# Kernel optimization log

Hardware: AMD Instinct MI355X
Metric: run time of the kernel (lower is better)

The kernel has to match this reference:

```python
import jax, jax.numpy as jnp
import numpy as np

B, R, T, F_IN, L, D, H, OUT, ES = 8, 128, 64, 32, 64, 64, 128, 32, 2048
DT = 0.1  # dt_step from init


def _glorot(key, shape):
    scale = 1.0 / np.sqrt(shape[0])
    return (jax.random.normal(key, shape, jnp.float32) * scale).astype(jnp.float32)


def setup_inputs() -> dict:
    key = jax.random.key(0)
    ks = jax.random.split(key, 20)
    return {
        "node_feats": jax.random.normal(ks[0], (B, R, T, F_IN), jnp.float32),
        "eps": jax.random.normal(ks[1], (B, R, L + D), jnp.float32),
        "space_w": jax.random.uniform(ks[2], (B, ES), jnp.float32),
        "src": jax.random.randint(ks[3], (ES,), 0, R, jnp.int32),
        "dst": jax.random.randint(ks[4], (ES,), 0, R, jnp.int32),
        "W_e1": _glorot(ks[5], (F_IN + 1, H)),
        "b_e1": jnp.zeros((H,), jnp.float32),
        "W_e2": _glorot(ks[6], (H, H)),
        "b_e2": jnp.zeros((H,), jnp.float32),
        "W_mu": _glorot(ks[7], (H, L + D)),
        "W_sig": _glorot(ks[8], (H, L + D)),
        "W_msg": _glorot(ks[9], (L, L)),
        "W_self": _glorot(ks[10], (L, L)),
        "W_dyn": _glorot(ks[11], (D, L)),
        "b_ode": jnp.zeros((L,), jnp.float32),
        "W_d1": _glorot(ks[12], (L + D + 1 + R, H)),
        "b_d1": jnp.zeros((H,), jnp.float32),
        "W_d2": _glorot(ks[13], (H, OUT)),
        "b_d2": jnp.zeros((OUT,), jnp.float32),
    }


def reference(node_feats, eps, space_w, src, dst,
              W_e1, b_e1, W_e2, b_e2, W_mu, W_sig,
              W_msg, W_self, W_dyn, b_ode,
              W_d1, b_d1, W_d2, b_d2):
    dt = jnp.asarray(DT, node_feats.dtype)
    tgrid = jnp.arange(T, dtype=node_feats.dtype) / T  # normalized time, like t/t.max()
    t_feat = jnp.broadcast_to(tgrid[None, None, :, None], (B, R, T, 1))

    # ---- Encoder: node features + time -> per-node mu/sigma (NP-style) ----
    x = jnp.concatenate([node_feats, t_feat], axis=-1)          # [B,R,T,F+1]
    h = jax.nn.silu(x @ W_e1 + b_e1)
    h = jax.nn.silu(h @ W_e2 + b_e2)
    hp = h.mean(axis=2)                                          # pool over time -> [B,R,H]
    mu = hp @ W_mu                                               # [B,R,L+D]
    sigma = 0.1 + 0.9 * jax.nn.sigmoid(hp @ W_sig)
    v = mu + sigma * eps                                         # reparameterized latent
    Lz, Dz = v[..., :L], v[..., L:]                              # integrated state / h_dyn

    # ---- MPGCN ODE func: weighted edge gather/scatter + self + h_dyn ----
    dyn = Dz @ W_dyn                                             # constant conditioning [B,R,L]

    def f(xs):                                                   # xs: [B,R,L]
        m = space_w[..., None] * xs[:, src, :]                   # per-edge message [B,E,L]
        agg = jnp.zeros((B, R, L), xs.dtype).at[:, dst].add(m)   # sum aggregation
        return jnp.tanh(agg @ W_msg + xs @ W_self + dyn + b_ode)

    # ---- RK4 fixed-step integrator, save state at every time point ----
    def step(xs, _):
        k1 = f(xs)
        k2 = f(xs + 0.5 * dt * k1)
        k3 = f(xs + 0.5 * dt * k2)
        k4 = f(xs + dt * k3)
        xn = xs + (dt / 6.0) * (k1 + 2.0 * k2 + 2.0 * k3 + k4)
        return xn, xn

    _, traj = jax.lax.scan(step, Lz, None, length=T)             # [T,B,R,L]
    traj = jnp.moveaxis(traj, 0, 2)                              # [B,R,T,L]

    # ---- Decoder: [L(t), h_dyn, time, region one-hot] -> y ----
    rid = jnp.broadcast_to(jnp.eye(R, dtype=traj.dtype)[None, :, None, :], (B, R, T, R))
    d_rep = jnp.broadcast_to(Dz[:, :, None, :], (B, R, T, D))
    dec_in = jnp.concatenate([traj, d_rep, t_feat, rid], axis=-1)  # [B,R,T,257]
    hd = jax.nn.silu(dec_in @ W_d1 + b_d1)
    y = hd @ W_d2 + b_d2                                         # [B,R,T,OUT]
    return y
```

## Files before the change

### kernel.cpp

```cpp
#include <hip/hip_runtime.h>

#define B_ 8
#define R_ 128
#define T_ 64
#define FIN_ 32
#define L_ 64
#define D_ 64
#define H_ 128
#define OUT_ 32
#define ES_ 2048

typedef _Float16 f16;
typedef __attribute__((ext_vector_type(2))) _Float16 f16x2;
typedef __attribute__((ext_vector_type(4))) _Float16 f16x4;
typedef __attribute__((ext_vector_type(8))) _Float16 f16x8;
typedef __attribute__((ext_vector_type(16))) float f32x16;

__device__ __forceinline__ float silu_f(float x) { return x / (1.f + __expf(-x)); }
__device__ __forceinline__ float tanh_f(float x) {
    float e = __expf(2.f * x);
    return 1.f - 2.f / (e + 1.f);
}

__device__ __forceinline__ uint32_t swzP(uint32_t r, uint32_t cByte) {
    return (r * 256u + cByte) ^ ((r & 15u) << 4);
}
__device__ __forceinline__ uint32_t swz256(uint32_t row, uint32_t s, uint32_t colByte) {
    uint32_t bo = row * 256u + s * 128u + colByte;
    return bo ^ ((row & 15u) << 4);
}
__device__ __forceinline__ uint32_t swzT(uint32_t c, uint32_t s, uint32_t rByte) {
    uint32_t bo = c * 512u + s * 256u + rByte;
    return bo ^ ((c & 31u) << 4);
}

__device__ __forceinline__ uint32_t pack2_f16(f16 a, f16 b) {
    union { f16x2 h; uint32_t u; } r;
    r.h[0] = a; r.h[1] = b;
    return r.u;
}

#define XP_OFF   0u
#define MT_OFF   32768u
#define WS_OFF   65536u
#define WM_OFF   81920u
#define PRM_OFF  98304u
#define ODE_LDS  110592u

__global__ __launch_bounds__(256) void encoder_kernel(
    const float* __restrict__ node_feats, const float* __restrict__ eps,
    const float* __restrict__ W_e1, const float* __restrict__ b_e1,
    const float* __restrict__ W_e2, const float* __restrict__ b_e2,
    const float* __restrict__ W_mu, const float* __restrict__ W_sig,
    const float* __restrict__ W_dyn,
    float* __restrict__ Lz, float* __restrict__ Dz, float* __restrict__ dynb) {
    int br = blockIdx.x;
    int tid = threadIdx.x;
    __shared__ __align__(16) float xS[T_ * 36];
    __shared__ __align__(16) float h1[T_ * H_];
    __shared__ float hps[2 * H_];
    __shared__ float hp[H_];
    __shared__ float muS[H_], sgS[H_], vS[H_];

    const float* nf = node_feats + (size_t)br * (T_ * FIN_);
    for (int i = tid; i < T_ * FIN_; i += 256) {
        int t = i >> 5, f = i & 31;
        xS[t * 36 + f] = nf[i];
    }
    if (tid < T_) xS[tid * 36 + 32] = (float)tid * (1.f / 64.f);

    int j = tid & 127;
    int th = tid >> 7;
    float we1r[33];
    #pragma unroll
    for (int k = 0; k < 33; ++k) we1r[k] = W_e1[k * H_ + j];
    __syncthreads();

    float be1 = b_e1[j];
    for (int tt = 0; tt < 32; ++tt) {
        int t = th * 32 + tt;
        float a = be1;
        const float4* xr = (const float4*)(&xS[t * 36]);
        #pragma unroll
        for (int w4 = 0; w4 < 8; ++w4) {
            float4 xv = xr[w4];
            a += xv.x * we1r[w4 * 4 + 0] + xv.y * we1r[w4 * 4 + 1] +
                 xv.z * we1r[w4 * 4 + 2] + xv.w * we1r[w4 * 4 + 3];
        }
        a += xS[t * 36 + 32] * we1r[32];
        h1[t * H_ + j] = silu_f(a);
    }
    __syncthreads();

    float acc[32];
    float be2 = b_e2[j];
    #pragma unroll
    for (int tt = 0; tt < 32; ++tt) acc[tt] = be2;
    for (int kc = 0; kc < 4; ++kc) {
        float wreg[32];
        #pragma unroll
        for (int i2 = 0; i2 < 32; ++i2) wreg[i2] = W_e2[(kc * 32 + i2) * H_ + j];
        #pragma unroll
        for (int tt = 0; tt < 32; ++tt) {
            int t = th * 32 + tt;
            const float4* hrow = (const float4*)(&h1[t * H_ + kc * 32]);
            float s = 0.f;
            #pragma unroll
            for (int w4 = 0; w4 < 8; ++w4) {
                float4 hv = hrow[w4];
                s += hv.x * wreg[w4 * 4 + 0] + hv.y * wreg[w4 * 4 + 1] +
                     hv.z * wreg[w4 * 4 + 2] + hv.w * wreg[w4 * 4 + 3];
            }
            acc[tt] += s;
        }
    }
    float msum = 0.f;
    #pragma unroll
    for (int tt = 0; tt < 32; ++tt) msum += silu_f(acc[tt]);
    hps[th * H_ + j] = msum;
    __syncthreads();
    if (tid < H_) hp[tid] = (hps[tid] + hps[H_ + tid]) * (1.f / 64.f);
    __syncthreads();

    {
        const float* Wm = (th == 0) ? W_mu : W_sig;
        float a = 0.f;
        #pragma unroll 4
        for (int k = 0; k < H_; ++k) a += hp[k] * Wm[k * H_ + j];
        if (th == 0) muS[j] = a; else sgS[j] = a;
    }
    __syncthreads();
    if (tid < H_) {
        float sig = 0.1f + 0.9f / (1.f + __expf(-sgS[tid]));
        float v = muS[tid] + sig * eps[(size_t)br * H_ + tid];
        vS[tid] = v;
        if (tid < L_) Lz[(size_t)br * L_ + tid] = v;
        else          Dz[(size_t)br * D_ + (tid - L_)] = v;
    }
    __syncthreads();
    if (tid < L_) {
        float a = 0.f;
        #pragma unroll 4
        for (int k = 0; k < D_; ++k) a += vS[L_ + k] * W_dyn[k * L_ + tid];
        dynb[(size_t)br * L_ + tid] = a;
    }
}

__global__ __launch_bounds__(512, 2) void ode_kernel(
    const float* __restrict__ Lz, const float* __restrict__ dynb,
    const float* __restrict__ W_msg, const float* __restrict__ W_self,
    const float* __restrict__ b_ode,
    const int* __restrict__ src, const int* __restrict__ dst,
    const float* __restrict__ space_w,
    float* __restrict__ traj) {
    const int b = blockIdx.x;
    const int tid = threadIdx.x;
    const int lane = tid & 63;
    const int w = tid >> 6;
    const int rb = w & 3;
    const int cb = w >> 2;
    const int l31 = lane & 31;
    const int h = lane >> 5;
    const int cc = cb * 32 + l31;

    extern __shared__ char sm[];
    float* Af  = (float*)sm;
    int* permS = (int*)(sm + PRM_OFF);
    int* cnt4  = permS + ES_;
    int* cntS  = cnt4 + 512;
    int* rsS   = cntS + R_;

    for (int idx = tid; idx < 4096; idx += 512) {
        int j = idx & 63, k = idx >> 6;
        float vs = W_self[k * 64 + j];
        f16 sh = (f16)vs;
        *(f16*)(sm + WS_OFF + swz256(j, 0, k * 2)) = sh;
        *(f16*)(sm + WS_OFF + swz256(j, 1, k * 2)) = (f16)(vs - (float)sh);
        float vm = W_msg[k * 64 + j];
        f16 mh = (f16)vm;
        *(f16*)(sm + WM_OFF + swz256(j, 0, k * 2)) = mh;
        *(f16*)(sm + WM_OFF + swz256(j, 1, k * 2)) = (f16)(vm - (float)mh);
    }

    {
        const int c4 = tid >> 7;
        const int rr = tid & 127;
        int c = 0;
        const int eb = c4 * 512;
        for (int e = eb; e < eb + 512; ++e) c += (dst[e] == rr) ? 1 : 0;
        cnt4[c4 * 128 + rr] = c;
    }
    __syncthreads();
    if (tid < R_)
        cntS[tid] = cnt4[tid] + cnt4[128 + tid] + cnt4[256 + tid] + cnt4[384 + tid];
    __syncthreads();
    if (tid == 0) {
        int a = 0;
        for (int i = 0; i < R_; ++i) { rsS[i] = a; a += cntS[i]; }
        rsS[R_] = a;
    }
    __syncthreads();
    {
        const int c4 = tid >> 7;
        const int rr = tid & 127;
        int k = rsS[rr];
        for (int c = 0; c < c4; ++c) k += cnt4[c * 128 + rr];
        const int eb = c4 * 512;
        for (int e = eb; e < eb + 512; ++e)
            if (dst[e] == rr) permS[k++] = e;
    }
    for (int i = tid; i < 128 * 128; i += 512) Af[i] = 0.f;
    __syncthreads();
    if (tid < R_) {
        int e0_ = rsS[tid], e1_ = rsS[tid + 1];
        for (int e = e0_; e < e1_; ++e) {
            int pe = permS[e];
            Af[tid * 128 + src[pe]] += space_w[b * ES_ + pe];
        }
    }
    __syncthreads();

    f16x8 aH[8], aL[8];
    {
        int row = rb * 32 + l31;
        #pragma unroll
        for (int m = 0; m < 8; ++m) {
            const float* p = Af + row * 128 + m * 16 + h * 8;
            f16x8 vh, vl;
            #pragma unroll
            for (int i = 0; i < 8; ++i) {
                float v = p[i];
                f16 hi = (f16)v;
                vh[i] = hi;
                vl[i] = (f16)(v - (float)hi);
            }
            aH[m] = vh;
            aL[m] = vl;
        }
    }

    float xb[16], ks[16], dnb[16];
    {
        float bo = b_ode[cc];
        #pragma unroll
        for (int i = 0; i < 16; ++i) {
            int r = rb * 32 + (i & 3) + 8 * (i >> 2) + 4 * h;
            size_t o = ((size_t)(b * R_ + r)) * L_ + cc;
            xb[i] = Lz[o];
            dnb[i] = dynb[o] + bo;
        }
    }
    __syncthreads();

    #pragma unroll
    for (int i = 0; i < 16; ++i) {
        int r = rb * 32 + (i & 3) + 8 * (i >> 2) + 4 * h;
        f16 hi = (f16)xb[i];
        *(uint32_t*)(sm + XP_OFF + swzP(r, (uint32_t)cc * 4u)) =
            pack2_f16(hi, (f16)(xb[i] - (float)hi));
    }
    __syncthreads();

    const int rowx = rb * 32 + l31;

    for (int n = 0; n < T_; ++n) {
        #pragma unroll
        for (int i = 0; i < 16; ++i) ks[i] = 0.f;
        for (int s4 = 0; s4 < 4; ++s4) {
            const float wk = (s4 == 1 || s4 == 2) ? 2.f : 1.f;
            const float cn = (s4 < 2) ? 0.05f : 0.1f;

            f16x8 xh[4], xl[4];
            #pragma unroll
            for (int m = 0; m < 4; ++m) {
                uint32_t cB = (uint32_t)(m * 16 + 8 * h) * 4u;
                uint4 p0 = *(const uint4*)(sm + XP_OFF + swzP(rowx, cB));
                uint4 p1 = *(const uint4*)(sm + XP_OFF + swzP(rowx, cB + 16u));
                union { uint32_t u[4]; f16x8 v; } H, L;
                H.u[0] = __builtin_amdgcn_perm(p0.y, p0.x, 0x05040100u);
                H.u[1] = __builtin_amdgcn_perm(p0.w, p0.z, 0x05040100u);
                H.u[2] = __builtin_amdgcn_perm(p1.y, p1.x, 0x05040100u);
                H.u[3] = __builtin_amdgcn_perm(p1.w, p1.z, 0x05040100u);
                L.u[0] = __builtin_amdgcn_perm(p0.y, p0.x, 0x07060302u);
                L.u[1] = __builtin_amdgcn_perm(p0.w, p0.z, 0x07060302u);
                L.u[2] = __builtin_amdgcn_perm(p1.y, p1.x, 0x07060302u);
                L.u[3] = __builtin_amdgcn_perm(p1.w, p1.z, 0x07060302u);
                xh[m] = H.v; xl[m] = L.v;
            }
            f32x16 aS, aM = {};
            #pragma unroll
            for (int i = 0; i < 16; ++i) aS[i] = dnb[i];
            #pragma unroll
            for (int m = 0; m < 4; ++m) {
                uint32_t kB = (m * 16 + 8 * h) * 2;
                f16x8 wsH = *(const f16x8*)(sm + WS_OFF + swz256(cc, 0, kB));
                f16x8 wsL = *(const f16x8*)(sm + WS_OFF + swz256(cc, 1, kB));
                f16x8 wmH = *(const f16x8*)(sm + WM_OFF + swz256(cc, 0, kB));
                f16x8 wmL = *(const f16x8*)(sm + WM_OFF + swz256(cc, 1, kB));
                aS = __builtin_amdgcn_mfma_f32_32x32x16_f16(xh[m], wsH, aS, 0, 0, 0);
                aM = __builtin_amdgcn_mfma_f32_32x32x16_f16(xh[m], wmH, aM, 0, 0, 0);
                aS = __builtin_amdgcn_mfma_f32_32x32x16_f16(xl[m], wsH, aS, 0, 0, 0);
                aM = __builtin_amdgcn_mfma_f32_32x32x16_f16(xl[m], wmH, aM, 0, 0, 0);
                aS = __builtin_amdgcn_mfma_f32_32x32x16_f16(xh[m], wsL, aS, 0, 0, 0);
                aM = __builtin_amdgcn_mfma_f32_32x32x16_f16(xh[m], wmL, aM, 0, 0, 0);
            }
            #pragma unroll
            for (int q = 0; q < 4; ++q) {
                int rbase = rb * 32 + 8 * q + 4 * h;
                f16x4 vh, vl;
                #pragma unroll
                for (int u = 0; u < 4; ++u) {
                    float t = aM[4 * q + u];
                    f16 hi = (f16)t;
                    vh[u] = hi;
                    vl[u] = (f16)(t - (float)hi);
                }
                *(f16x4*)(sm + MT_OFF + swzT(cc, 0, rbase * 2)) = vh;
                *(f16x4*)(sm + MT_OFF + swzT(cc, 1, rbase * 2)) = vl;
            }
            __syncthreads();

            f32x16 e0 = {}, e1 = {}, e2 = {};
            #pragma unroll
            for (int m = 0; m < 8; ++m) {
                f16x8 mtH = *(const f16x8*)(sm + MT_OFF + swzT(cc, 0, (m * 16 + 8 * h) * 2));
                f16x8 mtL = *(const f16x8*)(sm + MT_OFF + swzT(cc, 1, (m * 16 + 8 * h) * 2));
                if (m < 3) {
                    e0 = __builtin_amdgcn_mfma_f32_32x32x16_f16(aH[m], mtH, e0, 0, 0, 0);
                    e0 = __builtin_amdgcn_mfma_f32_32x32x16_f16(aL[m], mtH, e0, 0, 0, 0);
                    e0 = __builtin_amdgcn_mfma_f32_32x32x16_f16(aH[m], mtL, e0, 0, 0, 0);
                } else if (m < 6) {
                    e1 = __builtin_amdgcn_mfma_f32_32x32x16_f16(aH[m], mtH, e1, 0, 0, 0);
                    e1 = __builtin_amdgcn_mfma_f32_32x32x16_f16(aL[m], mtH, e1, 0, 0, 0);
                    e1 = __builtin_amdgcn_mfma_f32_32x32x16_f16(aH[m], mtL, e1, 0, 0, 0);
                } else {
                    e2 = __builtin_amdgcn_mfma_f32_32x32x16_f16(aH[m], mtH, e2, 0, 0, 0);
                    e2 = __builtin_amdgcn_mfma_f32_32x32x16_f16(aL[m], mtH, e2, 0, 0, 0);
                    e2 = __builtin_amdgcn_mfma_f32_32x32x16_f16(aH[m], mtL, e2, 0, 0, 0);
                }
            }
            float xn_[16];
            #pragma unroll
            for (int i = 0; i < 16; ++i) {
                float kv = tanh_f(aS[i] + e0[i] + e1[i] + e2[i]);
                ks[i] += wk * kv;
                xn_[i] = (s4 < 3) ? (xb[i] + cn * kv) : (xb[i] + (0.1f / 6.f) * ks[i]);
            }
            if (s4 == 3) {
                #pragma unroll
                for (int i = 0; i < 16; ++i) xb[i] = xn_[i];
            }
            #pragma unroll
            for (int i = 0; i < 16; ++i) {
                int r = rb * 32 + (i & 3) + 8 * (i >> 2) + 4 * h;
                f16 hi = (f16)xn_[i];
                *(uint32_t*)(sm + XP_OFF + swzP(r, (uint32_t)cc * 4u)) =
                    pack2_f16(hi, (f16)(xn_[i] - (float)hi));
            }
            if (s4 == 3) {
                #pragma unroll
                for (int i = 0; i < 16; ++i) {
                    int r = rb * 32 + (i & 3) + 8 * (i >> 2) + 4 * h;
                    traj[(((size_t)b * T_ + n) * R_ + r) * L_ + cc] = xb[i];
                }
            }
            __syncthreads();
        }
    }
}

__global__ __launch_bounds__(256) void decoder_kernel(
    const float* __restrict__ traj, const float* __restrict__ Dz,
    const float* __restrict__ W_d1, const float* __restrict__ b_d1,
    const float* __restrict__ W_d2, const float* __restrict__ b_d2,
    float* __restrict__ y) {
    int br = blockIdx.x;
    int b = br >> 7;
    int r = br & 127;
    int tid = threadIdx.x;
    __shared__ __align__(16) float trajS[32 * L_];
    __shared__ __align__(16) float hS[32 * H_];
    __shared__ float dzS[D_];
    __shared__ float baseS[H_];

    int j = tid & 127;
    int th = tid >> 7;
    if (tid < D_) dzS[tid] = Dz[(size_t)br * D_ + tid];
    __syncthreads();

    float wcol[64];
    #pragma unroll
    for (int k = 0; k < 64; ++k) wcol[k] = W_d1[k * H_ + j];
    float wt = W_d1[128 * H_ + j];
    if (th == 0) {
        float a = b_d1[j] + W_d1[(129 + r) * H_ + j];
        #pragma unroll 4
        for (int k = 0; k < D_; ++k) a += dzS[k] * W_d1[(64 + k) * H_ + j];
        baseS[j] = a;
    }
    __syncthreads();
    float bb = baseS[j];

    for (int half = 0; half < 2; ++half) {
        for (int i = tid; i < 32 * L_; i += 256) {
            int tt = i >> 6, l = i & 63;
            trajS[i] = traj[(((size_t)b * T_ + half * 32 + tt) * R_ + r) * L_ + l];
        }
        __syncthreads();
        #pragma unroll
        for (int tt = 0; tt < 16; ++tt) {
            int tl = th * 16 + tt;
            int t = half * 32 + tl;
            float a = bb + (float)t * (1.f / 64.f) * wt;
            const float4* tr4 = (const float4*)(&trajS[tl * L_]);
            #pragma unroll
            for (int kb = 0; kb < 16; ++kb) {
                float4 tv = tr4[kb];
                a += tv.x * wcol[kb * 4 + 0] + tv.y * wcol[kb * 4 + 1] +
                     tv.z * wcol[kb * 4 + 2] + tv.w * wcol[kb * 4 + 3];
            }
            hS[tl * H_ + j] = silu_f(a);
        }
        __syncthreads();
        {
            int o = tid & 31, q = tid >> 5;
            float acc2[4];
            float bd2 = b_d2[o];
            #pragma unroll
            for (int u = 0; u < 4; ++u) acc2[u] = bd2;
            for (int jc = 0; jc < 4; ++jc) {
                float wreg[32];
                #pragma unroll
                for (int i2 = 0; i2 < 32; ++i2) wreg[i2] = W_d2[(jc * 32 + i2) * OUT_ + o];
                #pragma unroll
                for (int u = 0; u < 4; ++u) {
                    int tl = q * 4 + u;
                    const float4* h4 = (const float4*)(&hS[tl * H_ + jc * 32]);
                    float s2 = 0.f;
                    #pragma unroll
                    for (int w4 = 0; w4 < 8; ++w4) {
                        float4 hv = h4[w4];
                        s2 += hv.x * wreg[w4 * 4 + 0] + hv.y * wreg[w4 * 4 + 1] +
                              hv.z * wreg[w4 * 4 + 2] + hv.w * wreg[w4 * 4 + 3];
                    }
                    acc2[u] += s2;
                }
            }
            #pragma unroll
            for (int u = 0; u < 4; ++u) {
                int t = half * 32 + q * 4 + u;
                y[((size_t)br * T_ + t) * OUT_ + o] = acc2[u];
            }
        }
        __syncthreads();
    }
}

extern "C" void kernel_launch(void* const* d_in, const int* in_sizes, int n_in,
                              void* d_out, int out_size, void* d_ws, size_t ws_size,
                              hipStream_t stream) {
    const float* node_feats = (const float*)d_in[0];
    const float* eps_       = (const float*)d_in[1];
    const float* space_w    = (const float*)d_in[2];
    const int*   src        = (const int*)d_in[3];
    const int*   dst        = (const int*)d_in[4];
    const float* W_e1 = (const float*)d_in[5];
    const float* b_e1 = (const float*)d_in[6];
    const float* W_e2 = (const float*)d_in[7];
    const float* b_e2 = (const float*)d_in[8];
    const float* W_mu = (const float*)d_in[9];
    const float* W_sig = (const float*)d_in[10];
    const float* W_msg = (const float*)d_in[11];
    const float* W_self = (const float*)d_in[12];
    const float* W_dyn = (const float*)d_in[13];
    const float* b_ode = (const float*)d_in[14];
    const float* W_d1 = (const float*)d_in[15];
    const float* b_d1 = (const float*)d_in[16];
    const float* W_d2 = (const float*)d_in[17];
    const float* b_d2 = (const float*)d_in[18];
    float* out = (float*)d_out;

    float* f_ws = (float*)d_ws;
    float* Lz    = f_ws;
    float* Dz    = Lz + B_ * R_ * L_;
    float* dynb  = Dz + B_ * R_ * D_;
    float* traj  = dynb + B_ * R_ * L_;

    encoder_kernel<<<B_ * R_, 256, 0, stream>>>(node_feats, eps_, W_e1, b_e1, W_e2, b_e2,
                                                W_mu, W_sig, W_dyn, Lz, Dz, dynb);
    ode_kernel<<<B_, 512, ODE_LDS, stream>>>(Lz, dynb, W_msg, W_self, b_ode,
                                             src, dst, space_w, traj);
    decoder_kernel<<<B_ * R_, 256, 0, stream>>>(traj, Dz, W_d1, b_d1, W_d2, b_d2, out);
}
```

Measured before the change: 1.449 ms.

## Register-tile encoder MLP and interleave hi/lo f16 message storage in LDS

Each thread in the encoder now computes a 4-column by 8-timestep register tile with float4 weight loads, instead of one column over 32 timesteps. This increases reuse of both weights and inputs and makes the global weight loads vectorized and coalesced. In the ODE kernel, the hi and lo f16 halves of the message matrix are stored interleaved as one 16-byte write rather than two 8-byte writes, and are split back with byte-permute instructions after 16-byte reads. This trades extra ALU perm work for fewer and wider LDS accesses.

```diff
diff --git a/kernel.cpp b/kernel.cpp
--- a/kernel.cpp
+++ b/kernel.cpp
@@ -29,9 +29,8 @@
     uint32_t bo = row * 256u + s * 128u + colByte;
     return bo ^ ((row & 15u) << 4);
 }
-__device__ __forceinline__ uint32_t swzT(uint32_t c, uint32_t s, uint32_t rByte) {
-    uint32_t bo = c * 512u + s * 256u + rByte;
-    return bo ^ ((c & 31u) << 4);
+__device__ __forceinline__ uint32_t swzTP(uint32_t c, uint32_t rByte) {
+    return (c * 512u + rByte) ^ ((c & 31u) << 4);
 }
 
 __device__ __forceinline__ uint32_t pack2_f16(f16 a, f16 b) {
@@ -58,7 +57,7 @@
     int tid = threadIdx.x;
     __shared__ __align__(16) float xS[T_ * 36];
     __shared__ __align__(16) float h1[T_ * H_];
-    __shared__ float hps[2 * H_];
+    __shared__ float hps2[8][H_];
     __shared__ float hp[H_];
     __shared__ float muS[H_], sgS[H_], vS[H_];
 
@@ -68,61 +67,103 @@
         xS[t * 36 + f] = nf[i];
     }
     if (tid < T_) xS[tid * 36 + 32] = (float)tid * (1.f / 64.f);
-
-    int j = tid & 127;
-    int th = tid >> 7;
-    float we1r[33];
-    #pragma unroll
-    for (int k = 0; k < 33; ++k) we1r[k] = W_e1[k * H_ + j];
-    __syncthreads();
-
-    float be1 = b_e1[j];
-    for (int tt = 0; tt < 32; ++tt) {
-        int t = th * 32 + tt;
-        float a = be1;
-        const float4* xr = (const float4*)(&xS[t * 36]);
-        #pragma unroll
-        for (int w4 = 0; w4 < 8; ++w4) {
-            float4 xv = xr[w4];
-            a += xv.x * we1r[w4 * 4 + 0] + xv.y * we1r[w4 * 4 + 1] +
-                 xv.z * we1r[w4 * 4 + 2] + xv.w * we1r[w4 * 4 + 3];
-        }
-        a += xS[t * 36 + 32] * we1r[32];
-        h1[t * H_ + j] = silu_f(a);
-    }
-    __syncthreads();
-
-    float acc[32];
-    float be2 = b_e2[j];
-    #pragma unroll
-    for (int tt = 0; tt < 32; ++tt) acc[tt] = be2;
-    for (int kc = 0; kc < 4; ++kc) {
-        float wreg[32];
-        #pragma unroll
-        for (int i2 = 0; i2 < 32; ++i2) wreg[i2] = W_e2[(kc * 32 + i2) * H_ + j];
-        #pragma unroll
-        for (int tt = 0; tt < 32; ++tt) {
-            int t = th * 32 + tt;
-            const float4* hrow = (const float4*)(&h1[t * H_ + kc * 32]);
+    __syncthreads();
+
+    const int jg = tid & 31;
+    const int th8 = tid >> 5;
+    const int j0 = jg * 4;
+    const int t0 = th8 * 8;
+
+    float acc1[8][4];
+    {
+        float4 bv = *(const float4*)&b_e1[j0];
+        #pragma unroll
+        for (int t = 0; t < 8; ++t) {
+            acc1[t][0] = bv.x; acc1[t][1] = bv.y; acc1[t][2] = bv.z; acc1[t][3] = bv.w;
+        }
+        #pragma unroll
+        for (int kb = 0; kb < 4; ++kb) {
+            const int k0 = kb * 8;
+            float4 wr[8];
+            #pragma unroll
+            for (int i = 0; i < 8; ++i) wr[i] = *(const float4*)&W_e1[(k0 + i) * H_ + j0];
+            #pragma unroll
+            for (int t = 0; t < 8; ++t) {
+                const float* xrow = &xS[(t0 + t) * 36 + k0];
+                float4 xa = *(const float4*)xrow;
+                float4 xc = *(const float4*)(xrow + 4);
+                #pragma unroll
+                for (int jj = 0; jj < 4; ++jj) {
+                    float wj0 = (&wr[0].x)[jj], wj1 = (&wr[1].x)[jj], wj2 = (&wr[2].x)[jj], wj3 = (&wr[3].x)[jj];
+                    float wj4 = (&wr[4].x)[jj], wj5 = (&wr[5].x)[jj], wj6 = (&wr[6].x)[jj], wj7 = (&wr[7].x)[jj];
+                    acc1[t][jj] += xa.x * wj0 + xa.y * wj1 + xa.z * wj2 + xa.w * wj3 +
+                                   xc.x * wj4 + xc.y * wj5 + xc.z * wj6 + xc.w * wj7;
+                }
+            }
+        }
+        float4 w32 = *(const float4*)&W_e1[32 * H_ + j0];
+        #pragma unroll
+        for (int t = 0; t < 8; ++t) {
+            float xv = xS[(t0 + t) * 36 + 32];
+            acc1[t][0] += xv * w32.x; acc1[t][1] += xv * w32.y;
+            acc1[t][2] += xv * w32.z; acc1[t][3] += xv * w32.w;
+        }
+        #pragma unroll
+        for (int t = 0; t < 8; ++t) {
+            float4 o;
+            o.x = silu_f(acc1[t][0]); o.y = silu_f(acc1[t][1]);
+            o.z = silu_f(acc1[t][2]); o.w = silu_f(acc1[t][3]);
+            *(float4*)&h1[(t0 + t) * H_ + j0] = o;
+        }
+    }
+    __syncthreads();
+
+    {
+        float acc[8][4];
+        float4 bv = *(const float4*)&b_e2[j0];
+        #pragma unroll
+        for (int t = 0; t < 8; ++t) {
+            acc[t][0] = bv.x; acc[t][1] = bv.y; acc[t][2] = bv.z; acc[t][3] = bv.w;
+        }
+        for (int kb = 0; kb < 16; ++kb) {
+            const int k0 = kb * 8;
+            float4 wr[8];
+            #pragma unroll
+            for (int i = 0; i < 8; ++i) wr[i] = *(const float4*)&W_e2[(k0 + i) * H_ + j0];
+            #pragma unroll
+            for (int t = 0; t < 8; ++t) {
+                const float4* hrow = (const float4*)&h1[(t0 + t) * H_ + k0];
+                float4 ha = hrow[0];
+                float4 hc = hrow[1];
+                #pragma unroll
+                for (int jj = 0; jj < 4; ++jj) {
+                    float wj0 = (&wr[0].x)[jj], wj1 = (&wr[1].x)[jj], wj2 = (&wr[2].x)[jj], wj3 = (&wr[3].x)[jj];
+                    float wj4 = (&wr[4].x)[jj], wj5 = (&wr[5].x)[jj], wj6 = (&wr[6].x)[jj], wj7 = (&wr[7].x)[jj];
+                    acc[t][jj] += ha.x * wj0 + ha.y * wj1 + ha.z * wj2 + ha.w * wj3 +
+                                  hc.x * wj4 + hc.y * wj5 + hc.z * wj6 + hc.w * wj7;
+                }
+            }
+        }
+        #pragma unroll
+        for (int jj = 0; jj < 4; ++jj) {
             float s = 0.f;
             #pragma unroll
-            for (int w4 = 0; w4 < 8; ++w4) {
-                float4 hv = hrow[w4];
-                s += hv.x * wreg[w4 * 4 + 0] + hv.y * wreg[w4 * 4 + 1] +
-                     hv.z * wreg[w4 * 4 + 2] + hv.w * wreg[w4 * 4 + 3];
-            }
-            acc[tt] += s;
-        }
-    }
-    float msum = 0.f;
-    #pragma unroll
-    for (int tt = 0; tt < 32; ++tt) msum += silu_f(acc[tt]);
-    hps[th * H_ + j] = msum;
-    __syncthreads();
-    if (tid < H_) hp[tid] = (hps[tid] + hps[H_ + tid]) * (1.f / 64.f);
-    __syncthreads();
-
-    {
+            for (int t = 0; t < 8; ++t) s += silu_f(acc[t][jj]);
+            hps2[th8][j0 + jj] = s;
+        }
+    }
+    __syncthreads();
+    if (tid < H_) {
+        float s = 0.f;
+        #pragma unroll
+        for (int g = 0; g < 8; ++g) s += hps2[g][tid];
+        hp[tid] = s * (1.f / 64.f);
+    }
+    __syncthreads();
+
+    {
+        int j = tid & 127;
+        int th = tid >> 7;
         const float* Wm = (th == 0) ? W_mu : W_sig;
         float a = 0.f;
         #pragma unroll 4
@@ -307,24 +348,36 @@
             #pragma unroll
             for (int q = 0; q < 4; ++q) {
                 int rbase = rb * 32 + 8 * q + 4 * h;
-                f16x4 vh, vl;
-                #pragma unroll
-                for (int u = 0; u < 4; ++u) {
-                    float t = aM[4 * q + u];
-                    f16 hi = (f16)t;
-                    vh[u] = hi;
-                    vl[u] = (f16)(t - (float)hi);
+                uint4 pk;
+                {
+                    float v0 = aM[4 * q + 0], v1 = aM[4 * q + 1];
+                    float v2 = aM[4 * q + 2], v3 = aM[4 * q + 3];
+                    f16 h0 = (f16)v0, h1_ = (f16)v1, h2 = (f16)v2, h3 = (f16)v3;
+                    pk.x = pack2_f16(h0, (f16)(v0 - (float)h0));
+                    pk.y = pack2_f16(h1_, (f16)(v1 - (float)h1_));
+                    pk.z = pack2_f16(h2, (f16)(v2 - (float)h2));
+                    pk.w = pack2_f16(h3, (f16)(v3 - (float)h3));
                 }
-                *(f16x4*)(sm + MT_OFF + swzT(cc, 0, rbase * 2)) = vh;
-                *(f16x4*)(sm + MT_OFF + swzT(cc, 1, rbase * 2)) = vl;
+                *(uint4*)(sm + MT_OFF + swzTP(cc, (uint32_t)rbase * 4u)) = pk;
             }
             __syncthreads();
 
             f32x16 e0 = {}, e1 = {}, e2 = {};
             #pragma unroll
             for (int m = 0; m < 8; ++m) {
-                f16x8 mtH = *(const f16x8*)(sm + MT_OFF + swzT(cc, 0, (m * 16 + 8 * h) * 2));
-                f16x8 mtL = *(const f16x8*)(sm + MT_OFF + swzT(cc, 1, (m * 16 + 8 * h) * 2));
+                uint32_t rB = (uint32_t)(m * 16 + 8 * h) * 4u;
+                uint4 p0 = *(const uint4*)(sm + MT_OFF + swzTP(cc, rB));
+                uint4 p1 = *(const uint4*)(sm + MT_OFF + swzTP(cc, rB + 16u));
+                union { uint32_t u[4]; f16x8 v; } H, L;
+                H.u[0] = __builtin_amdgcn_perm(p0.y, p0.x, 0x05040100u);
+                H.u[1] = __builtin_amdgcn_perm(p0.w, p0.z, 0x05040100u);
+                H.u[2] = __builtin_amdgcn_perm(p1.y, p1.x, 0x05040100u);
+                H.u[3] = __builtin_amdgcn_perm(p1.w, p1.z, 0x05040100u);
+                L.u[0] = __builtin_amdgcn_perm(p0.y, p0.x, 0x07060302u);
+                L.u[1] = __builtin_amdgcn_perm(p0.w, p0.z, 0x07060302u);
+                L.u[2] = __builtin_amdgcn_perm(p1.y, p1.x, 0x07060302u);
+                L.u[3] = __builtin_amdgcn_perm(p1.w, p1.z, 0x07060302u);
+                f16x8 mtH = H.v, mtL = L.v;
                 if (m < 3) {
                     e0 = __builtin_amdgcn_mfma_f32_32x32x16_f16(aH[m], mtH, e0, 0, 0, 0);
                     e0 = __builtin_amdgcn_mfma_f32_32x32x16_f16(aL[m], mtH, e0, 0, 0, 0);
```

After: 1.421 ms. No clear change (-1.9%).
